# Performance work log

Measured on AMD Instinct MI355X. Metric: run time of the kernel, lower is better.

The kernel has to match this reference:

```python
import jax, jax.numpy as jnp
import numpy as np

D_MODEL = 768
NUM_HEADS = 12
D_K = D_MODEL // NUM_HEADS


def setup_inputs() -> dict:
    key = jax.random.key(0)
    ks = jax.random.split(key, 11)
    B, L = 1, 4096
    s = 1.0 / np.sqrt(D_MODEL)
    return {
        "q": jax.random.normal(ks[0], (B, L, D_MODEL), jnp.float32),
        "k": jax.random.normal(ks[1], (B, L, D_MODEL), jnp.float32),
        "v": jax.random.normal(ks[2], (B, L, D_MODEL), jnp.float32),
        "Wq": jax.random.normal(ks[3], (D_MODEL, D_MODEL), jnp.float32) * s,
        "bq": jax.random.normal(ks[4], (D_MODEL,), jnp.float32) * s,
        "Wk": jax.random.normal(ks[5], (D_MODEL, D_MODEL), jnp.float32) * s,
        "bk": jax.random.normal(ks[6], (D_MODEL,), jnp.float32) * s,
        "Wv": jax.random.normal(ks[7], (D_MODEL, D_MODEL), jnp.float32) * s,
        "bv": jax.random.normal(ks[8], (D_MODEL,), jnp.float32) * s,
        "Wo": jax.random.normal(ks[9], (D_MODEL, D_MODEL), jnp.float32) * s,
        "bo": jax.random.normal(ks[10], (D_MODEL,), jnp.float32) * s,
    }


def reference(q, k, v, Wq, bq, Wk, bk, Wv, bv, Wo, bo):
    B, L, _ = q.shape
    # linear projections (torch Linear: x @ W.T + b)
    qp = q @ Wq.T + bq
    kp = k @ Wk.T + bk
    vp = v @ Wv.T + bv
    # split heads: (B, H, L, d_k)
    def split(x):
        return x.reshape(B, L, NUM_HEADS, D_K).transpose(0, 2, 1, 3)
    qh, kh, vh = split(qp), split(kp), split(vp)
    scale = 1.0 / jnp.sqrt(jnp.asarray(D_K, qh.dtype))
    scores = jnp.einsum("bhqd,bhkd->bhqk", qh, kh) * scale  # (B,H,L,L)
    weights = jax.nn.softmax(scores, axis=-1)
    out = jnp.einsum("bhqk,bhkd->bhqd", weights, vh)
    out = out.transpose(0, 2, 1, 3).reshape(B, L, D_MODEL)
    return out @ Wo.T + bo
```

## Files before the change

### kernel.cpp

```cpp
#include <hip/hip_runtime.h>
#include <stdint.h>
#include <math.h>

#define L_SEQ  4096
#define DMODEL 768
#define NHEADS 12
#define DKH    64
#define QSCALE 0.18033688011112042f

typedef _Float16 f16;
typedef __attribute__((ext_vector_type(8))) _Float16 half8;
typedef __attribute__((ext_vector_type(4))) _Float16 half4;
typedef __attribute__((ext_vector_type(4))) float f32x4;
typedef __attribute__((ext_vector_type(16))) float f32x16;
typedef __attribute__((ext_vector_type(4))) unsigned int uint4v;

#define MFMA16(a, b, c) __builtin_amdgcn_mfma_f32_16x16x32_f16(a, b, c, 0, 0, 0)
#define MFMA32(a, b, c) __builtin_amdgcn_mfma_f32_32x32x16_f16(a, b, c, 0, 0, 0)

#define NE ((size_t)L_SEQ * DMODEL)
#define WE ((size_t)DMODEL * DMODEL)

static __device__ __forceinline__ unsigned int pack2(float a, float b) {
  return __builtin_bit_cast(unsigned int, __builtin_amdgcn_cvt_pkrtz(a, b));
}

__global__ __launch_bounds__(256)
void cvt_all(const float* __restrict__ q, const float* __restrict__ k,
             const float* __restrict__ v, const float* __restrict__ Wq,
             const float* __restrict__ Wk, const float* __restrict__ Wv,
             const float* __restrict__ Wo, f16* __restrict__ x16,
             f16* __restrict__ w16)
{
  const size_t NE4 = NE / 4, WE4 = WE / 4;
  size_t i = (size_t)blockIdx.x * 256 + threadIdx.x;
  const float* srcs[7] = {q, k, v, Wq, Wk, Wv, Wo};
  f16* dsts[7] = {x16, x16 + NE, x16 + 2 * NE,
                  w16, w16 + WE, w16 + 2 * WE, w16 + 3 * WE};
  const size_t sz4[7] = {NE4, NE4, NE4, WE4, WE4, WE4, WE4};
  int r = 0; size_t off = i;
  while (off >= sz4[r]) { off -= sz4[r]; ++r; }
  float4 f = reinterpret_cast<const float4*>(srcs[r])[off];
  half4 h; h[0] = (f16)f.x; h[1] = (f16)f.y; h[2] = (f16)f.z; h[3] = (f16)f.w;
  reinterpret_cast<half4*>(dsts[r])[off] = h;
}

__global__ __launch_bounds__(256)
void qkv_gemm(const f16* __restrict__ x16, const f16* __restrict__ w16,
              const float* __restrict__ bq, const float* __restrict__ bk,
              const float* __restrict__ bv,
              f16* __restrict__ Qp, f16* __restrict__ Kp, f16* __restrict__ VpT)
{
  __shared__ f16 As[128][40];
  __shared__ f16 Bs[64][40];
  const int tid  = threadIdx.x;
  const int lane = tid & 63, wid = tid >> 6;
  const int lq   = lane & 15, quad = lane >> 4;
  const int wm   = (wid & 1) * 64, wn = (wid >> 1) * 32;
  const int m0   = blockIdx.y * 128;
  const int widx = blockIdx.x / 12;
  const int n0   = (blockIdx.x % 12) * 64;
  const f16* X = x16 + (size_t)widx * NE;
  const f16* W = w16 + (size_t)widx * WE;
  const float* Bv = (widx == 0) ? bq : (widx == 1) ? bk : bv;

  const int arow = tid >> 1, aseg = (tid & 1) * 16;
  const int brow = tid >> 2, bseg = (tid & 3) * 8;
  const f16* aptr = X + (size_t)(m0 + arow) * DMODEL + aseg;
  const f16* bptr = W + (size_t)(n0 + brow) * DMODEL + bseg;

  half8 a0 = *reinterpret_cast<const half8*>(aptr);
  half8 a1 = *reinterpret_cast<const half8*>(aptr + 8);
  half8 b0 = *reinterpret_cast<const half8*>(bptr);

  f32x4 acc[4][2] = {};

  for (int k0 = 0; k0 < DMODEL; k0 += 32) {
    *reinterpret_cast<half8*>(&As[arow][aseg])     = a0;
    *reinterpret_cast<half8*>(&As[arow][aseg + 8]) = a1;
    *reinterpret_cast<half8*>(&Bs[brow][bseg])     = b0;
    __syncthreads();

    if (k0 + 32 < DMODEL) {
      a0 = *reinterpret_cast<const half8*>(aptr + k0 + 32);
      a1 = *reinterpret_cast<const half8*>(aptr + k0 + 40);
      b0 = *reinterpret_cast<const half8*>(bptr + k0 + 32);
    }

    half8 bf[2];
#pragma unroll
    for (int nf = 0; nf < 2; ++nf)
      bf[nf] = *reinterpret_cast<half8*>(&Bs[wn + nf * 16 + lq][quad * 8]);
#pragma unroll
    for (int mf = 0; mf < 4; ++mf) {
      half8 af = *reinterpret_cast<half8*>(&As[wm + mf * 16 + lq][quad * 8]);
#pragma unroll
      for (int nf = 0; nf < 2; ++nf)
        acc[mf][nf] = MFMA16(af, bf[nf], acc[mf][nf]);
    }
    __syncthreads();
  }

#pragma unroll
  for (int nf = 0; nf < 2; ++nf) {
    const int col  = n0 + wn + nf * 16 + lq;
    const float bias = Bv[col];
#pragma unroll
    for (int mf = 0; mf < 4; ++mf) {
      const int rowb = m0 + wm + mf * 16 + quad * 4;
      if (widx == 2) {
        half4 o4;
#pragma unroll
        for (int r = 0; r < 4; ++r) o4[r] = (f16)(acc[mf][nf][r] + bias);
        *reinterpret_cast<half4*>(VpT + (size_t)col * L_SEQ + rowb) = o4;
      } else if (widx == 0) {
#pragma unroll
        for (int r = 0; r < 4; ++r)
          Qp[(size_t)(rowb + r) * DMODEL + col] = (f16)((acc[mf][nf][r] + bias) * QSCALE);
      } else {
#pragma unroll
        for (int r = 0; r < 4; ++r)
          Kp[(size_t)(rowb + r) * DMODEL + col] = (f16)(acc[mf][nf][r] + bias);
      }
    }
  }
}

__global__ __launch_bounds__(256, 3)
void attn_mfma4(const f16* __restrict__ Qp, const f16* __restrict__ Kp,
                const f16* __restrict__ VpT, f16* __restrict__ AO)
{
  const int h  = blockIdx.x;
  const int q0 = blockIdx.y * 64;
  const int tid  = threadIdx.x;
  const int lane = tid & 63, wid = tid >> 6;
  const int l31  = lane & 31, hc = lane >> 5;
  const int qh   = wid & 1, kh = wid >> 1;

  __shared__ __align__(16) char smem[25088];
  f16 (*Ks)[72] = (f16 (*)[72])smem;
  f16 (*Vt)[72] = (f16 (*)[72])(smem + 9216);
  float* Of  = (float*)smem;
  float* lf  = (float*)(smem + 16384);
  f16*   Of16 = (f16*)(smem + 16640);

  half8 qf[4];
#pragma unroll
  for (int st = 0; st < 4; ++st)
    qf[st] = *reinterpret_cast<const half8*>(
        Qp + (size_t)(q0 + qh * 32 + l31) * DMODEL + h * DKH + st * 16 + hc * 8);

  f32x16 oacc[2] = {};
  float lsum = 0.0f;

  const int srow = tid >> 2, sseg = (tid & 3) * 16;
  const f16* kbase = Kp  + (size_t)srow * DMODEL + h * DKH + sseg;
  const f16* vbase = VpT + (size_t)(h * DKH + srow) * L_SEQ + sseg;

  half8 k0 = *reinterpret_cast<const half8*>(kbase);
  half8 k1 = *reinterpret_cast<const half8*>(kbase + 8);
  half8 v0 = *reinterpret_cast<const half8*>(vbase);
  half8 v1 = *reinterpret_cast<const half8*>(vbase + 8);

  for (int kt = 0; kt < L_SEQ; kt += 64) {
    *reinterpret_cast<half8*>(&Ks[srow][sseg])     = k0;
    *reinterpret_cast<half8*>(&Ks[srow][sseg + 8]) = k1;
    *reinterpret_cast<half8*>(&Vt[srow][sseg])     = v0;
    *reinterpret_cast<half8*>(&Vt[srow][sseg + 8]) = v1;
    __syncthreads();

    if (kt + 64 < L_SEQ) {
      const f16* kn = kbase + (size_t)(kt + 64) * DMODEL;
      const f16* vn = vbase + (kt + 64);
      k0 = *reinterpret_cast<const half8*>(kn);
      k1 = *reinterpret_cast<const half8*>(kn + 8);
      v0 = *reinterpret_cast<const half8*>(vn);
      v1 = *reinterpret_cast<const half8*>(vn + 8);
    }

    f32x16 s = {};
#pragma unroll
    for (int st = 0; st < 4; ++st) {
      half8 kf = *reinterpret_cast<half8*>(&Ks[kh * 32 + l31][st * 16 + hc * 8]);
      s = MFMA32(kf, qf[st], s);
    }

    unsigned int pk[8];
#pragma unroll
    for (int i = 0; i < 8; ++i) {
      float p0 = exp2f(s[2 * i]);
      float p1 = exp2f(s[2 * i + 1]);
      lsum += p0 + p1;
      pk[i] = pack2(p0, p1);
    }

    unsigned int recv[4];
#pragma unroll
    for (int j = 0; j < 4; ++j) {
      unsigned int sv = hc ? pk[(j & 1) + 4 * (j >> 1)]
                           : pk[2 + (j & 1) + 4 * (j >> 1)];
      recv[j] = (unsigned int)__shfl_xor((int)sv, 32);
    }

#pragma unroll
    for (int st = 0; st < 2; ++st) {
      uint4v pw;
#pragma unroll
      for (int t = 0; t < 4; ++t) {
        unsigned int h0v = (t < 2) ? pk[(t & 1) + 4 * st] : recv[2 * st + (t & 1)];
        unsigned int h1v = (t < 2) ? recv[2 * st + (t & 1)] : pk[(t & 1) + 4 * st + 2];
        pw[t] = hc ? h1v : h0v;
      }
      half8 pf = __builtin_bit_cast(half8, pw);
#pragma unroll
      for (int a = 0; a < 2; ++a) {
        half8 vf = *reinterpret_cast<half8*>(&Vt[a * 32 + l31][kh * 32 + st * 16 + hc * 8]);
        oacc[a] = MFMA32(vf, pf, oacc[a]);
      }
    }
    __syncthreads();
  }

  float lw = lsum + __shfl_xor(lsum, 32);

  if (kh == 0) {
#pragma unroll
    for (int a = 0; a < 2; ++a)
#pragma unroll
      for (int r = 0; r < 16; ++r) {
        int d = a * 32 + (r & 3) + 8 * (r >> 2) + 4 * hc;
        Of[((qh * 64) + d) * 32 + l31] = oacc[a][r];
      }
    if (lane < 32) lf[qh * 32 + l31] = lw;
  }
  __syncthreads();
  if (kh == 1) {
    const float inv = 1.0f / (lf[qh * 32 + l31] + lw);
#pragma unroll
    for (int a = 0; a < 2; ++a)
#pragma unroll
      for (int r = 0; r < 16; ++r) {
        int d = a * 32 + (r & 3) + 8 * (r >> 2) + 4 * hc;
        float val = (Of[((qh * 64) + d) * 32 + l31] + oacc[a][r]) * inv;
        Of16[(qh * 32 + l31) * 64 + d] = (f16)val;
      }
  }
  __syncthreads();

  *reinterpret_cast<half8*>(AO + (size_t)(q0 + srow) * DMODEL + h * DKH + sseg) =
      *reinterpret_cast<half8*>(&Of16[srow * 64 + sseg]);
  *reinterpret_cast<half8*>(AO + (size_t)(q0 + srow) * DMODEL + h * DKH + sseg + 8) =
      *reinterpret_cast<half8*>(&Of16[srow * 64 + sseg + 8]);
}

__global__ __launch_bounds__(256)
void out_gemm(const f16* __restrict__ A, const f16* __restrict__ W,
              const float* __restrict__ Bv, float* __restrict__ O)
{
  __shared__ f16 As[64][72];
  __shared__ f16 Bs[64][72];
  const int tid  = threadIdx.x;
  const int lane = tid & 63, wid = tid >> 6;
  const int lq   = lane & 15, quad = lane >> 4;
  const int wm   = (wid & 1) * 32, wn = (wid >> 1) * 32;
  const int m0   = blockIdx.y * 64, n0 = blockIdx.x * 64;

  const int row = tid >> 2, seg = (tid & 3) * 16;
  const f16* aptr = A + (size_t)(m0 + row) * DMODEL + seg;
  const f16* bptr = W + (size_t)(n0 + row) * DMODEL + seg;

  half8 a0 = *reinterpret_cast<const half8*>(aptr);
  half8 a1 = *reinterpret_cast<const half8*>(aptr + 8);
  half8 b0 = *reinterpret_cast<const half8*>(bptr);
  half8 b1 = *reinterpret_cast<const half8*>(bptr + 8);

  f32x4 acc[2][2] = {};

  for (int k0 = 0; k0 < DMODEL; k0 += 64) {
    *reinterpret_cast<half8*>(&As[row][seg])     = a0;
    *reinterpret_cast<half8*>(&As[row][seg + 8]) = a1;
    *reinterpret_cast<half8*>(&Bs[row][seg])     = b0;
    *reinterpret_cast<half8*>(&Bs[row][seg + 8]) = b1;
    __syncthreads();

    if (k0 + 64 < DMODEL) {
      a0 = *reinterpret_cast<const half8*>(aptr + k0 + 64);
      a1 = *reinterpret_cast<const half8*>(aptr + k0 + 72);
      b0 = *reinterpret_cast<const half8*>(bptr + k0 + 64);
      b1 = *reinterpret_cast<const half8*>(bptr + k0 + 72);
    }

#pragma unroll
    for (int ks = 0; ks < 2; ++ks) {
      half8 bf[2];
#pragma unroll
      for (int nf = 0; nf < 2; ++nf)
        bf[nf] = *reinterpret_cast<half8*>(&Bs[wn + nf * 16 + lq][ks * 32 + quad * 8]);
#pragma unroll
      for (int mf = 0; mf < 2; ++mf) {
        half8 af = *reinterpret_cast<half8*>(&As[wm + mf * 16 + lq][ks * 32 + quad * 8]);
#pragma unroll
        for (int nf = 0; nf < 2; ++nf)
          acc[mf][nf] = MFMA16(af, bf[nf], acc[mf][nf]);
      }
    }
    __syncthreads();
  }

#pragma unroll
  for (int nf = 0; nf < 2; ++nf) {
    const int col = n0 + wn + nf * 16 + lq;
    const float bias = Bv[col];
#pragma unroll
    for (int mf = 0; mf < 2; ++mf) {
      const int rowb = m0 + wm + mf * 16 + quad * 4;
#pragma unroll
      for (int r = 0; r < 4; ++r)
        O[(size_t)(rowb + r) * DMODEL + col] = acc[mf][nf][r] + bias;
    }
  }
}

extern "C" void kernel_launch(void* const* d_in, const int* in_sizes, int n_in,
                              void* d_out, int out_size, void* d_ws, size_t ws_size,
                              hipStream_t stream) {
  const float* q  = (const float*)d_in[0];
  const float* k  = (const float*)d_in[1];
  const float* v  = (const float*)d_in[2];
  const float* Wq = (const float*)d_in[3];
  const float* bq = (const float*)d_in[4];
  const float* Wk = (const float*)d_in[5];
  const float* bk = (const float*)d_in[6];
  const float* Wv = (const float*)d_in[7];
  const float* bv = (const float*)d_in[8];
  const float* Wo = (const float*)d_in[9];
  const float* bo = (const float*)d_in[10];
  float* out = (float*)d_out;

  f16* x16 = (f16*)d_ws;
  f16* w16 = x16 + 3 * NE;
  f16* Qp  = w16 + 4 * WE;
  f16* Kp  = Qp + NE;
  f16* VpT = Kp + NE;
  f16* AO  = VpT + NE;

  const int ncvt = (int)((3 * (NE / 4) + 4 * (WE / 4)) / 256);
  cvt_all<<<ncvt, 256, 0, stream>>>(q, k, v, Wq, Wk, Wv, Wo, x16, w16);

  dim3 gqkv(36, L_SEQ / 128);
  qkv_gemm<<<gqkv, 256, 0, stream>>>(x16, w16, bq, bk, bv, Qp, Kp, VpT);

  dim3 gattn(NHEADS, L_SEQ / 64);
  attn_mfma4<<<gattn, 256, 0, stream>>>(Qp, Kp, VpT, AO);

  dim3 gout(DMODEL / 64, L_SEQ / 64);
  out_gemm<<<gout, 256, 0, stream>>>(AO, w16 + 3 * WE, bo, out);
}
```

Before: 246.2 us.

## Unify projection GEMMs into 128x128 tiled kernel using 32x32 MFMA

Replaces the separate QKV and output projection GEMMs with one templated kernel. It uses 128x128 block tiles, a K step of 64 and 32x32x16 MFMA instructions. The goal is more data reuse per shared-memory load and fewer instructions per FLOP. The trade-off is fewer blocks, especially for the output GEMM at 192 blocks, which may underfill the GPU, plus higher register and LDS use per block.

```diff
diff --git a/kernel.cpp b/kernel.cpp
--- a/kernel.cpp
+++ b/kernel.cpp
@@ -45,82 +45,118 @@
   reinterpret_cast<half4*>(dsts[r])[off] = h;
 }
 
+template<int KIND>
 __global__ __launch_bounds__(256)
-void qkv_gemm(const f16* __restrict__ x16, const f16* __restrict__ w16,
+void gemm_big(const f16* __restrict__ Abase, const f16* __restrict__ Wbase,
               const float* __restrict__ bq, const float* __restrict__ bk,
               const float* __restrict__ bv,
-              f16* __restrict__ Qp, f16* __restrict__ Kp, f16* __restrict__ VpT)
+              f16* __restrict__ Qp, f16* __restrict__ Kp, f16* __restrict__ VpT,
+              float* __restrict__ Ofp)
 {
-  __shared__ f16 As[128][40];
-  __shared__ f16 Bs[64][40];
+  __shared__ f16 As[128][72];
+  __shared__ f16 Bs[128][72];
   const int tid  = threadIdx.x;
   const int lane = tid & 63, wid = tid >> 6;
-  const int lq   = lane & 15, quad = lane >> 4;
-  const int wm   = (wid & 1) * 64, wn = (wid >> 1) * 32;
+  const int l31  = lane & 31, hc = lane >> 5;
+  const int wm   = (wid & 1) * 64, wn = (wid >> 1) * 64;
   const int m0   = blockIdx.y * 128;
-  const int widx = blockIdx.x / 12;
-  const int n0   = (blockIdx.x % 12) * 64;
-  const f16* X = x16 + (size_t)widx * NE;
-  const f16* W = w16 + (size_t)widx * WE;
-  const float* Bv = (widx == 0) ? bq : (widx == 1) ? bk : bv;
-
-  const int arow = tid >> 1, aseg = (tid & 1) * 16;
-  const int brow = tid >> 2, bseg = (tid & 3) * 8;
-  const f16* aptr = X + (size_t)(m0 + arow) * DMODEL + aseg;
-  const f16* bptr = W + (size_t)(n0 + brow) * DMODEL + bseg;
-
-  half8 a0 = *reinterpret_cast<const half8*>(aptr);
-  half8 a1 = *reinterpret_cast<const half8*>(aptr + 8);
-  half8 b0 = *reinterpret_cast<const half8*>(bptr);
-
-  f32x4 acc[4][2] = {};
-
-  for (int k0 = 0; k0 < DMODEL; k0 += 32) {
-    *reinterpret_cast<half8*>(&As[arow][aseg])     = a0;
-    *reinterpret_cast<half8*>(&As[arow][aseg + 8]) = a1;
-    *reinterpret_cast<half8*>(&Bs[brow][bseg])     = b0;
+
+  int widx, n0;
+  const f16 *A, *W;
+  if (KIND == 0) {
+    widx = blockIdx.x / 6;
+    n0   = (blockIdx.x % 6) * 128;
+    A = Abase + (size_t)widx * NE;
+    W = Wbase + (size_t)widx * WE;
+  } else {
+    widx = 3;
+    n0   = blockIdx.x * 128;
+    A = Abase;
+    W = Wbase;
+  }
+
+  const int srow = tid >> 1, sseg = (tid & 1) * 32;
+  const f16* aptr = A + (size_t)(m0 + srow) * DMODEL + sseg;
+  const f16* bptr = W + (size_t)(n0 + srow) * DMODEL + sseg;
+
+  half8 ar[4], br[4];
+#pragma unroll
+  for (int t = 0; t < 4; ++t) {
+    ar[t] = *reinterpret_cast<const half8*>(aptr + t * 8);
+    br[t] = *reinterpret_cast<const half8*>(bptr + t * 8);
+  }
+
+  f32x16 acc[2][2] = {};
+
+  for (int k0 = 0; k0 < DMODEL; k0 += 64) {
+#pragma unroll
+    for (int t = 0; t < 4; ++t) {
+      *reinterpret_cast<half8*>(&As[srow][sseg + t * 8]) = ar[t];
+      *reinterpret_cast<half8*>(&Bs[srow][sseg + t * 8]) = br[t];
+    }
     __syncthreads();
 
-    if (k0 + 32 < DMODEL) {
-      a0 = *reinterpret_cast<const half8*>(aptr + k0 + 32);
-      a1 = *reinterpret_cast<const half8*>(aptr + k0 + 40);
-      b0 = *reinterpret_cast<const half8*>(bptr + k0 + 32);
-    }
-
-    half8 bf[2];
-#pragma unroll
-    for (int nf = 0; nf < 2; ++nf)
-      bf[nf] = *reinterpret_cast<half8*>(&Bs[wn + nf * 16 + lq][quad * 8]);
-#pragma unroll
-    for (int mf = 0; mf < 4; ++mf) {
-      half8 af = *reinterpret_cast<half8*>(&As[wm + mf * 16 + lq][quad * 8]);
-#pragma unroll
-      for (int nf = 0; nf < 2; ++nf)
-        acc[mf][nf] = MFMA16(af, bf[nf], acc[mf][nf]);
+    if (k0 + 64 < DMODEL) {
+#pragma unroll
+      for (int t = 0; t < 4; ++t) {
+        ar[t] = *reinterpret_cast<const half8*>(aptr + k0 + 64 + t * 8);
+        br[t] = *reinterpret_cast<const half8*>(bptr + k0 + 64 + t * 8);
+      }
+    }
+
+#pragma unroll
+    for (int s = 0; s < 4; ++s) {
+      half8 af[2], bf[2];
+#pragma unroll
+      for (int a = 0; a < 2; ++a)
+        af[a] = *reinterpret_cast<half8*>(&As[wm + a * 32 + l31][s * 16 + hc * 8]);
+#pragma unroll
+      for (int b = 0; b < 2; ++b)
+        bf[b] = *reinterpret_cast<half8*>(&Bs[wn + b * 32 + l31][s * 16 + hc * 8]);
+#pragma unroll
+      for (int a = 0; a < 2; ++a)
+#pragma unroll
+        for (int b = 0; b < 2; ++b)
+          acc[a][b] = MFMA32(af[a], bf[b], acc[a][b]);
     }
     __syncthreads();
   }
 
 #pragma unroll
-  for (int nf = 0; nf < 2; ++nf) {
-    const int col  = n0 + wn + nf * 16 + lq;
-    const float bias = Bv[col];
-#pragma unroll
-    for (int mf = 0; mf < 4; ++mf) {
-      const int rowb = m0 + wm + mf * 16 + quad * 4;
-      if (widx == 2) {
-        half4 o4;
-#pragma unroll
-        for (int r = 0; r < 4; ++r) o4[r] = (f16)(acc[mf][nf][r] + bias);
-        *reinterpret_cast<half4*>(VpT + (size_t)col * L_SEQ + rowb) = o4;
+  for (int b = 0; b < 2; ++b) {
+    const int gn = n0 + wn + b * 32 + l31;
+    float bias;
+    if (KIND == 0) bias = (widx == 0) ? bq[gn] : (widx == 1) ? bk[gn] : bv[gn];
+    else           bias = bq[gn];
+#pragma unroll
+    for (int a = 0; a < 2; ++a) {
+      const int gmb = m0 + wm + a * 32 + 4 * hc;
+      if (KIND == 1) {
+#pragma unroll
+        for (int r = 0; r < 16; ++r) {
+          const int gm = gmb + (r & 3) + 8 * (r >> 2);
+          Ofp[(size_t)gm * DMODEL + gn] = acc[a][b][r] + bias;
+        }
+      } else if (widx == 2) {
+#pragma unroll
+        for (int g = 0; g < 4; ++g) {
+          half4 o4;
+#pragma unroll
+          for (int t = 0; t < 4; ++t) o4[t] = (f16)(acc[a][b][4 * g + t] + bias);
+          *reinterpret_cast<half4*>(VpT + (size_t)gn * L_SEQ + gmb + 8 * g) = o4;
+        }
       } else if (widx == 0) {
 #pragma unroll
-        for (int r = 0; r < 4; ++r)
-          Qp[(size_t)(rowb + r) * DMODEL + col] = (f16)((acc[mf][nf][r] + bias) * QSCALE);
+        for (int r = 0; r < 16; ++r) {
+          const int gm = gmb + (r & 3) + 8 * (r >> 2);
+          Qp[(size_t)gm * DMODEL + gn] = (f16)((acc[a][b][r] + bias) * QSCALE);
+        }
       } else {
 #pragma unroll
-        for (int r = 0; r < 4; ++r)
-          Kp[(size_t)(rowb + r) * DMODEL + col] = (f16)(acc[mf][nf][r] + bias);
+        for (int r = 0; r < 16; ++r) {
+          const int gm = gmb + (r & 3) + 8 * (r >> 2);
+          Kp[(size_t)gm * DMODEL + gn] = (f16)(acc[a][b][r] + bias);
+        }
       }
     }
   }
@@ -251,74 +287,6 @@
       *reinterpret_cast<half8*>(&Of16[srow * 64 + sseg]);
   *reinterpret_cast<half8*>(AO + (size_t)(q0 + srow) * DMODEL + h * DKH + sseg + 8) =
       *reinterpret_cast<half8*>(&Of16[srow * 64 + sseg + 8]);
-}
-
-__global__ __launch_bounds__(256)
-void out_gemm(const f16* __restrict__ A, const f16* __restrict__ W,
-              const float* __restrict__ Bv, float* __restrict__ O)
-{
-  __shared__ f16 As[64][72];
-  __shared__ f16 Bs[64][72];
-  const int tid  = threadIdx.x;
-  const int lane = tid & 63, wid = tid >> 6;
-  const int lq   = lane & 15, quad = lane >> 4;
-  const int wm   = (wid & 1) * 32, wn = (wid >> 1) * 32;
-  const int m0   = blockIdx.y * 64, n0 = blockIdx.x * 64;
-
-  const int row = tid >> 2, seg = (tid & 3) * 16;
-  const f16* aptr = A + (size_t)(m0 + row) * DMODEL + seg;
-  const f16* bptr = W + (size_t)(n0 + row) * DMODEL + seg;
-
-  half8 a0 = *reinterpret_cast<const half8*>(aptr);
-  half8 a1 = *reinterpret_cast<const half8*>(aptr + 8);
-  half8 b0 = *reinterpret_cast<const half8*>(bptr);
-  half8 b1 = *reinterpret_cast<const half8*>(bptr + 8);
-
-  f32x4 acc[2][2] = {};
-
-  for (int k0 = 0; k0 < DMODEL; k0 += 64) {
-    *reinterpret_cast<half8*>(&As[row][seg])     = a0;
-    *reinterpret_cast<half8*>(&As[row][seg + 8]) = a1;
-    *reinterpret_cast<half8*>(&Bs[row][seg])     = b0;
-    *reinterpret_cast<half8*>(&Bs[row][seg + 8]) = b1;
-    __syncthreads();
-
-    if (k0 + 64 < DMODEL) {
-      a0 = *reinterpret_cast<const half8*>(aptr + k0 + 64);
-      a1 = *reinterpret_cast<const half8*>(aptr + k0 + 72);
-      b0 = *reinterpret_cast<const half8*>(bptr + k0 + 64);
-      b1 = *reinterpret_cast<const half8*>(bptr + k0 + 72);
-    }
-
-#pragma unroll
-    for (int ks = 0; ks < 2; ++ks) {
-      half8 bf[2];
-#pragma unroll
-      for (int nf = 0; nf < 2; ++nf)
-        bf[nf] = *reinterpret_cast<half8*>(&Bs[wn + nf * 16 + lq][ks * 32 + quad * 8]);
-#pragma unroll
-      for (int mf = 0; mf < 2; ++mf) {
-        half8 af = *reinterpret_cast<half8*>(&As[wm + mf * 16 + lq][ks * 32 + quad * 8]);
-#pragma unroll
-        for (int nf = 0; nf < 2; ++nf)
-          acc[mf][nf] = MFMA16(af, bf[nf], acc[mf][nf]);
-      }
-    }
-    __syncthreads();
-  }
-
-#pragma unroll
-  for (int nf = 0; nf < 2; ++nf) {
-    const int col = n0 + wn + nf * 16 + lq;
-    const float bias = Bv[col];
-#pragma unroll
-    for (int mf = 0; mf < 2; ++mf) {
-      const int rowb = m0 + wm + mf * 16 + quad * 4;
-#pragma unroll
-      for (int r = 0; r < 4; ++r)
-        O[(size_t)(rowb + r) * DMODEL + col] = acc[mf][nf][r] + bias;
-    }
-  }
 }
 
 extern "C" void kernel_launch(void* const* d_in, const int* in_sizes, int n_in,
@@ -347,12 +315,14 @@
   const int ncvt = (int)((3 * (NE / 4) + 4 * (WE / 4)) / 256);
   cvt_all<<<ncvt, 256, 0, stream>>>(q, k, v, Wq, Wk, Wv, Wo, x16, w16);
 
-  dim3 gqkv(36, L_SEQ / 128);
-  qkv_gemm<<<gqkv, 256, 0, stream>>>(x16, w16, bq, bk, bv, Qp, Kp, VpT);
+  dim3 gqkv(18, L_SEQ / 128);
+  gemm_big<0><<<gqkv, 256, 0, stream>>>(x16, w16, bq, bk, bv,
+                                        Qp, Kp, VpT, nullptr);
 
   dim3 gattn(NHEADS, L_SEQ / 64);
   attn_mfma4<<<gattn, 256, 0, stream>>>(Qp, Kp, VpT, AO);
 
-  dim3 gout(DMODEL / 64, L_SEQ / 64);
-  out_gemm<<<gout, 256, 0, stream>>>(AO, w16 + 3 * WE, bo, out);
-}
+  dim3 gout(DMODEL / 128, L_SEQ / 128);
+  gemm_big<1><<<gout, 256, 0, stream>>>(AO, w16 + 3 * WE, bo, nullptr, nullptr,
+                                        nullptr, nullptr, nullptr, out);
+}
```

Measured after the change: 249.0 us. Within noise of the previous version (+1.1%).
